# Kernel tuning notes

Hardware: AMD Instinct MI355X
Metric: run time of the kernel (lower is better)

The kernel has to match this reference:

```python
import jax, jax.numpy as jnp
import numpy as np

CHEB_K = 2  # chebyshev polynomial order (support_ks = [I, A] for cheb_k=2)


def _fc(x, w1, b1, w2, b2, w3, b3):
    # FC module: Linear -> sigmoid -> Linear -> sigmoid -> Linear
    h = jax.nn.sigmoid(x @ w1 + b1)
    h = jax.nn.sigmoid(h @ w2 + b2)
    return h @ w3 + b3


def _preprocess(adj):
    # adj: [B,N,N]; add self-loops then row-normalize
    adj = adj + jnp.eye(adj.shape[-1], dtype=adj.dtype)
    return adj / adj.sum(-1, keepdims=True)


def _gcn(x, adjs, ne, wpool, bpool):
    # x: [B,N,C], adjs: list of [B,N,N], ne: [N,E]
    # wpool: [E, 2*CHEB_K, C, O], bpool: [E, O]
    mats = []
    for A in adjs:
        ks = [jnp.broadcast_to(jnp.eye(A.shape[-1], dtype=A.dtype), A.shape), A]
        for _ in range(2, CHEB_K):
            ks.append(2.0 * jnp.matmul(A, ks[-1]) - ks[-2])
        mats.extend(ks)
    # [B,N,K,C] with K = 2*CHEB_K
    x_g = jnp.stack([jnp.einsum('bnm,bmc->bnc', S, x) for S in mats], axis=2)
    weights = jnp.einsum('nd,dkio->nkio', ne, wpool)  # [N,K,C,O]
    bias = ne @ bpool  # [N,O]
    return jnp.einsum('bnki,nkio->bno', x_g, weights) + bias


def _forward(x, state, ne0, ne1, ne2, fc1_w1, fc1_b1, fc1_w2, fc1_b2, fc1_w3, fc1_b3,
             fc2_w1, fc2_b1, fc2_w2, fc2_b2, fc2_w3, fc2_b3, gate_w, gate_b, upd_w, upd_b):
    hid = upd_w.shape[-1]
    ins = jnp.concatenate([x, state], axis=-1)  # [B,N,dim_in+hid]
    f1 = _fc(ins, fc1_w1, fc1_b1, fc1_w2, fc1_b2, fc1_w3, fc1_b3)  # [B,N,TD]
    f2 = _fc(ins, fc2_w1, fc2_b1, fc2_w2, fc2_b2, fc2_w3, fc2_b3)
    nv1 = jnp.tanh(ne0[:, None, :] * f1)  # einsum 'bd,bnd->bnd' == broadcast mul
    nv2 = jnp.tanh(ne1[:, None, :] * f2)
    adj = jnp.einsum('bnd,bmd->bnm', nv1, nv2) - jnp.einsum('bnd,bmd->bnm', nv2, nv1)
    adj1 = _preprocess(jax.nn.relu(adj))
    adj2 = _preprocess(jax.nn.relu(-jnp.swapaxes(adj, -2, -1)))
    z_r = jax.nn.sigmoid(_gcn(ins, [adj1, adj2], ne2, gate_w, gate_b))
    z, r = z_r[..., :hid], z_r[..., hid:]
    cand = jnp.concatenate([x, z * state], axis=-1)
    hc = jnp.tanh(_gcn(cand, [adj1, adj2], ne2, upd_w, upd_b))
    return r * state + (1.0 - r) * hc


def setup_inputs():
    B, N, DIN, DOUT, ED, TD = 32, 1024, 2, 64, 10, 32
    HG, MID = 16, 2  # hyperGNN_dim, middle_dim hardcoded in FC
    CIN = DIN + DOUT
    K2 = 2 * CHEB_K
    ks = jax.random.split(jax.random.key(0), 16)
    rn = lambda i, shape, s=1.0: jax.random.normal(ks[i], shape, dtype=jnp.float32) * s
    return {
        'x': rn(0, (B, N, DIN)),
        'state': rn(1, (B, N, DOUT)),
        'ne0': rn(2, (B, TD)),
        'ne1': rn(3, (B, TD)),
        'ne2': rn(4, (N, ED), 0.1),
        'fc1_w1': rn(5, (CIN, HG), 0.1), 'fc1_b1': jnp.zeros((HG,), jnp.float32),
        'fc1_w2': rn(6, (HG, MID), 0.1), 'fc1_b2': jnp.zeros((MID,), jnp.float32),
        'fc1_w3': rn(7, (MID, TD), 0.1), 'fc1_b3': jnp.zeros((TD,), jnp.float32),
        'fc2_w1': rn(8, (CIN, HG), 0.1), 'fc2_b1': jnp.zeros((HG,), jnp.float32),
        'fc2_w2': rn(9, (HG, MID), 0.1), 'fc2_b2': jnp.zeros((MID,), jnp.float32),
        'fc2_w3': rn(10, (MID, TD), 0.1), 'fc2_b3': jnp.zeros((TD,), jnp.float32),
        'gate_w': rn(11, (ED, K2, CIN, 2 * DOUT), 0.1),
        'gate_b': rn(12, (ED, 2 * DOUT), 0.1),
        'upd_w': rn(13, (ED, K2, CIN, DOUT), 0.1),
        'upd_b': rn(14, (ED, DOUT), 0.1),
    }


def reference(x, state, ne0, ne1, ne2, fc1_w1, fc1_b1, fc1_w2, fc1_b2, fc1_w3, fc1_b3,
              fc2_w1, fc2_b1, fc2_w2, fc2_b2, fc2_w3, fc2_b3, gate_w, gate_b, upd_w, upd_b):
    return _forward(x, state, ne0, ne1, ne2, fc1_w1, fc1_b1, fc1_w2, fc1_b2, fc1_w3, fc1_b3,
                    fc2_w1, fc2_b1, fc2_w2, fc2_b2, fc2_w3, fc2_b3, gate_w, gate_b, upd_w, upd_b)
```

## Files before the change

kernel.cpp:

```cpp
#include <hip/hip_runtime.h>
#include <math.h>

#define BB   32
#define NN   1024
#define DIN  2
#define DOUT 64
#define CIN  66
#define TD   32
#define ED   10
#define OG   128
#define OU   64
#define KP   160
#define XTR  80

typedef __bf16 bf16x8 __attribute__((ext_vector_type(8)));
typedef float  f32x4  __attribute__((ext_vector_type(4)));
typedef short  s16x8  __attribute__((ext_vector_type(8)));

__device__ __forceinline__ unsigned short f2b(float f) {
    __bf16 h = (__bf16)f;
    return *(unsigned short*)&h;
}

__device__ __forceinline__ unsigned int cvt_pk_bf16(float lo, float hi) {
    unsigned int r;
    asm("v_cvt_pk_bf16_f32 %0, %1, %2" : "=v"(r) : "v"(lo), "v"(hi));
    return r;
}
__device__ __forceinline__ void perm32swap(unsigned int& a, unsigned int& b) {
    asm("v_permlane32_swap_b32 %0, %1" : "+v"(a), "+v"(b));
}
__device__ __forceinline__ void perm16swap(unsigned int& a, unsigned int& b) {
    asm("v_permlane16_swap_b32 %0, %1" : "+v"(a), "+v"(b));
}

__global__ __launch_bounds__(256) void k_pre(
    const float* __restrict__ x, const float* __restrict__ state,
    const float* __restrict__ ne0, const float* __restrict__ ne1,
    const float* __restrict__ ne2,
    const float* __restrict__ w11, const float* __restrict__ b11,
    const float* __restrict__ w12, const float* __restrict__ b12,
    const float* __restrict__ w13, const float* __restrict__ b13,
    const float* __restrict__ w21, const float* __restrict__ b21,
    const float* __restrict__ w22, const float* __restrict__ b22,
    const float* __restrict__ w23, const float* __restrict__ b23,
    const float* __restrict__ gate_w, const float* __restrict__ gate_b,
    const float* __restrict__ upd_w, const float* __restrict__ upd_b,
    unsigned short* __restrict__ nv1b, unsigned short* __restrict__ nv2b,
    unsigned short* __restrict__ XT0, unsigned short* __restrict__ XT1,
    unsigned short* __restrict__ BcTg, unsigned short* __restrict__ BcTu,
    float* __restrict__ biasG, float* __restrict__ biasU)
{
    __shared__ float sw[2408];
    __shared__ unsigned short st[68*72];
    int blk = blockIdx.x;
    int t = threadIdx.x;

    if (blk < 128) {
        const int oW1 = 0, oB1 = 1056, oW2 = 1072, oB2 = 1104, oW3 = 1108, oB3 = 1172, F2 = 1204;
        for (int i = t; i < 1056; i += 256) { sw[oW1+i] = w11[i]; sw[F2+oW1+i] = w21[i]; }
        if (t < 16) { sw[oB1+t] = b11[t]; sw[F2+oB1+t] = b21[t]; }
        if (t < 32) { sw[oW2+t] = w12[t]; sw[F2+oW2+t] = w22[t]; }
        if (t < 2)  { sw[oB2+t] = b12[t]; sw[F2+oB2+t] = b22[t]; }
        if (t < 64) { sw[oW3+t] = w13[t]; sw[F2+oW3+t] = w23[t]; }
        if (t >= 64 && t < 96) { sw[oB3+t-64] = b13[t-64]; sw[F2+oB3+t-64] = b23[t-64]; }
        __syncthreads();

        int p = blk*256 + t;
        int b = p >> 10;

        float h1a[16], h1b[16];
        #pragma unroll
        for (int j = 0; j < 16; ++j) { h1a[j] = sw[oB1+j]; h1b[j] = sw[F2+oB1+j]; }
        for (int i = 0; i < CIN; ++i) {
            float v = (i < DIN) ? x[(size_t)p*DIN + i] : state[(size_t)p*DOUT + (i-DIN)];
            #pragma unroll
            for (int jq = 0; jq < 4; ++jq) {
                float4 wa = *(const float4*)&sw[oW1 + i*16 + jq*4];
                float4 wb = *(const float4*)&sw[F2 + oW1 + i*16 + jq*4];
                h1a[jq*4+0] += v*wa.x; h1a[jq*4+1] += v*wa.y;
                h1a[jq*4+2] += v*wa.z; h1a[jq*4+3] += v*wa.w;
                h1b[jq*4+0] += v*wb.x; h1b[jq*4+1] += v*wb.y;
                h1b[jq*4+2] += v*wb.z; h1b[jq*4+3] += v*wb.w;
            }
        }
        #pragma unroll
        for (int j = 0; j < 16; ++j) {
            h1a[j] = 1.f/(1.f + __expf(-h1a[j]));
            h1b[j] = 1.f/(1.f + __expf(-h1b[j]));
        }
        float h2a0 = sw[oB2+0], h2a1 = sw[oB2+1];
        float h2b0 = sw[F2+oB2+0], h2b1 = sw[F2+oB2+1];
        #pragma unroll
        for (int i = 0; i < 16; ++i) {
            h2a0 += h1a[i]*sw[oW2 + i*2 + 0];
            h2a1 += h1a[i]*sw[oW2 + i*2 + 1];
            h2b0 += h1b[i]*sw[F2+oW2 + i*2 + 0];
            h2b1 += h1b[i]*sw[F2+oW2 + i*2 + 1];
        }
        h2a0 = 1.f/(1.f + __expf(-h2a0)); h2a1 = 1.f/(1.f + __expf(-h2a1));
        h2b0 = 1.f/(1.f + __expf(-h2b0)); h2b1 = 1.f/(1.f + __expf(-h2b1));

        const float* pn0 = ne0 + b*TD;
        const float* pn1 = ne1 + b*TD;
        #pragma unroll
        for (int jq = 0; jq < 8; ++jq) {
            float4 ba  = *(const float4*)&sw[oB3 + jq*4];
            float4 wa0 = *(const float4*)&sw[oW3 + jq*4];
            float4 wa1 = *(const float4*)&sw[oW3 + 32 + jq*4];
            float4 bb2 = *(const float4*)&sw[F2+oB3 + jq*4];
            float4 wb0 = *(const float4*)&sw[F2+oW3 + jq*4];
            float4 wb1 = *(const float4*)&sw[F2+oW3 + 32 + jq*4];
            float4 n0 = *(const float4*)&pn0[jq*4];
            float4 n1 = *(const float4*)&pn1[jq*4];
            ushort4 u1, u2;
            u1.x = f2b(tanhf(n0.x*(ba.x + h2a0*wa0.x + h2a1*wa1.x)));
            u1.y = f2b(tanhf(n0.y*(ba.y + h2a0*wa0.y + h2a1*wa1.y)));
            u1.z = f2b(tanhf(n0.z*(ba.z + h2a0*wa0.z + h2a1*wa1.z)));
            u1.w = f2b(tanhf(n0.w*(ba.w + h2a0*wa0.w + h2a1*wa1.w)));
            u2.x = f2b(tanhf(n1.x*(bb2.x + h2b0*wb0.x + h2b1*wb1.x)));
            u2.y = f2b(tanhf(n1.y*(bb2.y + h2b0*wb0.y + h2b1*wb1.y)));
            u2.z = f2b(tanhf(n1.z*(bb2.z + h2b0*wb0.z + h2b1*wb1.z)));
            u2.w = f2b(tanhf(n1.w*(bb2.w + h2b0*wb0.w + h2b1*wb1.w)));
            *(ushort4*)&nv1b[(size_t)p*TD + jq*4] = u1;
            *(ushort4*)&nv2b[(size_t)p*TD + jq*4] = u2;
        }
    } else if (blk < 640) {
        int idx = blk - 128;
        int b = idx >> 4, m0 = (idx & 15)*64;
        for (int i = t; i < 1024; i += 256) {
            int m = i >> 4, cq = i & 15;
            size_t base = (size_t)b*NN + m0 + m;
            float4 v = *(const float4*)&state[base*DOUT + cq*4];
            st[(2 + cq*4 + 0)*72 + m] = f2b(v.x);
            st[(2 + cq*4 + 1)*72 + m] = f2b(v.y);
            st[(2 + cq*4 + 2)*72 + m] = f2b(v.z);
            st[(2 + cq*4 + 3)*72 + m] = f2b(v.w);
        }
        if (t < 128) {
            int m = t >> 1, c = t & 1;
            st[c*72 + m] = f2b(x[((size_t)b*NN + m0 + m)*DIN + c]);
        }
        __syncthreads();
        const unsigned int ONE2 = 0x3F803F80u;
        for (int i = t; i < XTR*8; i += 256) {
            int c = i >> 3, ch = i & 7;
            uint4 v;
            if (c < 66)      v = *(const uint4*)&st[c*72 + ch*8];
            else if (c == 66) v = make_uint4(ONE2, ONE2, ONE2, ONE2);
            else              v = make_uint4(0, 0, 0, 0);
            *(uint4*)&XT0[((size_t)b*XTR + c)*NN + m0 + ch*8] = v;
            if (c < 2 || c >= 66)
                *(uint4*)&XT1[((size_t)b*XTR + c)*NN + m0 + ch*8] = v;
        }
    } else if (blk < 1840) {
        int tid = (blk - 640)*256 + t;
        int c = tid / KP, k = tid - c*KP;
        const float* pool; int O, cc; unsigned short* dst;
        if (c < 1280) { pool = gate_w; O = OG; cc = c;        dst = BcTg; }
        else          { pool = upd_w;  O = OU; cc = c - 1280; dst = BcTu; }
        int d = cc / O, o = cc - d*O;
        float v = 0.f;
        if (k < 132) {
            int kp = (k < 66) ? 0 : 1;
            int i  = (k < 66) ? k : k - 66;
            v = pool[(size_t)((d*4 + kp)*CIN + i)*O + o]
              + pool[(size_t)((d*4 + kp + 2)*CIN + i)*O + o];
        }
        dst[(size_t)cc*KP + k] = f2b(v);
    } else {
        int i = (blk - 1840)*256 + t;
        int n = i / 192, j = i - n*192;
        float v = 0.f;
        if (j < 128) {
            #pragma unroll
            for (int d = 0; d < ED; ++d) v += ne2[(size_t)n*ED + d]*gate_b[d*OG + j];
            biasG[(size_t)n*OG + j] = v;
        } else {
            int o = j - 128;
            #pragma unroll
            for (int d = 0; d < ED; ++d) v += ne2[(size_t)n*ED + d]*upd_b[d*OU + o];
            biasU[(size_t)n*OU + o] = v;
        }
    }
}

template<int O, int MODE>
__global__ __launch_bounds__(256) void k_fused(
    const unsigned short* __restrict__ nv1b, const unsigned short* __restrict__ nv2b,
    const unsigned short* __restrict__ XTg, const unsigned short* __restrict__ BcT,
    const float* __restrict__ ne2, const float* __restrict__ biasP,
    const float* __restrict__ state, unsigned short* __restrict__ XT1,
    float* __restrict__ rbuf, float* __restrict__ out)
{
    __shared__ unsigned short smem[24192];
    unsigned short* s_nv1c = smem;
    unsigned short* s_nv2c = smem + 5120;
    unsigned short* s_xt   = smem + 10240;

    int t = threadIdx.x;
    int id = blockIdx.x;
    int b = id & 31, rbase = (id >> 5)*64;
    int w = t >> 6, lane = t & 63, lq = lane >> 4, ln = lane & 15;

    bf16x8 a1 = *(const bf16x8*)&nv1b[((size_t)b*NN + rbase + 16*w + ln)*TD + lq*8];
    s16x8 a2s = *(const s16x8*)&nv2b[((size_t)b*NN + rbase + 16*w + ln)*TD + lq*8];
    const s16x8 sgn = {(short)0x8000,(short)0x8000,(short)0x8000,(short)0x8000,
                       (short)0x8000,(short)0x8000,(short)0x8000,(short)0x8000};
    a2s ^= sgn;
    bf16x8 a2n = (bf16x8)a2s;

    const unsigned short* pnv1 = nv1b + (size_t)b*NN*TD;
    const unsigned short* pnv2 = nv2b + (size_t)b*NN*TD;
    const unsigned short* pxt  = XTg  + (size_t)b*XTR*NN;
    int nnode = t >> 2;
    int nch   = (t & 3)*8;
    int xc    = t >> 3;
    int xch   = (t & 7)*8;

    uint4 q0, q1, r0, r1, r2;

    f32x4 acc[5];
    #pragma unroll
    for (int k = 0; k < 5; ++k) acc[k] = (f32x4){0.f,0.f,0.f,0.f};
    const f32x4 zero4 = {0.f,0.f,0.f,0.f};
    union U8 { unsigned int u[4]; bf16x8 v; };

    q0 = *(const uint4*)&pnv1[(size_t)nnode*TD + nch];
    q1 = *(const uint4*)&pnv2[(size_t)nnode*TD + nch];
    r0 = *(const uint4*)&pxt[(size_t)xc*NN + xch];
    r1 = *(const uint4*)&pxt[(size_t)(xc+32)*NN + xch];
    if (t < 128) r2 = *(const uint4*)&pxt[(size_t)(xc+64)*NN + xch];
    *(uint4*)&s_nv1c[nnode*40 + nch] = q0;
    *(uint4*)&s_nv2c[nnode*40 + nch] = q1;
    *(uint4*)&s_xt[xc*72 + xch] = r0;
    *(uint4*)&s_xt[(xc+32)*72 + xch] = r1;
    if (t < 128) *(uint4*)&s_xt[(xc+64)*72 + xch] = r2;
    q0 = *(const uint4*)&pnv1[(size_t)(64 + nnode)*TD + nch];
    q1 = *(const uint4*)&pnv2[(size_t)(64 + nnode)*TD + nch];
    r0 = *(const uint4*)&pxt[(size_t)xc*NN + 64 + xch];
    r1 = *(const uint4*)&pxt[(size_t)(xc+32)*NN + 64 + xch];
    if (t < 128) r2 = *(const uint4*)&pxt[(size_t)(xc+64)*NN + 64 + xch];
    __syncthreads();

    int cur = 0;
    for (int mb = 0; mb < NN; mb += 64) {
        if (mb + 64 < NN) {
            int nx = cur ^ 1;
            *(uint4*)&s_nv1c[nx*2560 + nnode*40 + nch] = q0;
            *(uint4*)&s_nv2c[nx*2560 + nnode*40 + nch] = q1;
            *(uint4*)&s_xt[nx*5760 + xc*72 + xch] = r0;
            *(uint4*)&s_xt[nx*5760 + (xc+32)*72 + xch] = r1;
            if (t < 128) *(uint4*)&s_xt[nx*5760 + (xc+64)*72 + xch] = r2;
        }
        if (mb + 128 < NN) {
            int mb2 = mb + 128;
            q0 = *(const uint4*)&pnv1[(size_t)(mb2 + nnode)*TD + nch];
            q1 = *(const uint4*)&pnv2[(size_t)(mb2 + nnode)*TD + nch];
            r0 = *(const uint4*)&pxt[(size_t)xc*NN + mb2 + xch];
            r1 = *(const uint4*)&pxt[(size_t)(xc+32)*NN + mb2 + xch];
            if (t < 128) r2 = *(const uint4*)&pxt[(size_t)(xc+64)*NN + mb2 + xch];
        }

        unsigned int u[4][2];
        #pragma unroll
        for (int jj = 0; jj < 4; ++jj) {
            bf16x8 b2 = *(const bf16x8*)&s_nv2c[cur*2560 + (jj*16 + ln)*40 + lq*8];
            bf16x8 b1 = *(const bf16x8*)&s_nv1c[cur*2560 + (jj*16 + ln)*40 + lq*8];
            f32x4 s = __builtin_amdgcn_mfma_f32_16x16x32_bf16(b2, a1,  zero4, 0, 0, 0);
            s       = __builtin_amdgcn_mfma_f32_16x16x32_bf16(b1, a2n, s,     0, 0, 0);
            u[jj][0] = cvt_pk_bf16(fmaxf(s[0], 0.f), fmaxf(s[1], 0.f));
            u[jj][1] = cvt_pk_bf16(fmaxf(s[2], 0.f), fmaxf(s[3], 0.f));
        }

        unsigned int w00 = u[0][0], w20 = u[1][0]; perm32swap(w00, w20); perm16swap(w00, w20);
        unsigned int w01 = u[0][1], w21 = u[1][1]; perm32swap(w01, w21); perm16swap(w01, w21);
        unsigned int x00 = u[2][0], x20 = u[3][0]; perm32swap(x00, x20); perm16swap(x00, x20);
        unsigned int x01 = u[2][1], x21 = u[3][1]; perm32swap(x01, x21); perm16swap(x01, x21);
        U8 p0, p1;
        p0.u[0] = w00; p0.u[1] = w01; p0.u[2] = w20; p0.u[3] = w21;
        p1.u[0] = x00; p1.u[1] = x01; p1.u[2] = x20; p1.u[3] = x21;
        bf16x8 pa0 = p0.v, pa1 = p1.v;

        #pragma unroll
        for (int k = 0; k < 5; ++k) {
            bf16x8 xb0 = *(const bf16x8*)&s_xt[cur*5760 + (k*16 + ln)*72 +      lq*8];
            bf16x8 xb1 = *(const bf16x8*)&s_xt[cur*5760 + (k*16 + ln)*72 + 32 + lq*8];
            acc[k] = __builtin_amdgcn_mfma_f32_16x16x32_bf16(pa0, xb0, acc[k], 0, 0, 0);
            acc[k] = __builtin_amdgcn_mfma_f32_16x16x32_bf16(pa1, xb1, acc[k], 0, 0, 0);
        }

        __syncthreads();
        cur ^= 1;
    }

    float rinv[4];
    #pragma unroll
    for (int r = 0; r < 4; ++r) {
        float rs = __shfl(acc[4][r], (lane & 48) | 2, 64);
        rinv[r] = 1.0f / (1.0f + rs);
    }

    unsigned short* s_A = smem;
    unsigned short* s_B = smem + 10752;

    for (int i = t; i < 64*28; i += 256) {
        int rr = i / 28, cc = 132 + (i - 28*(i/28));
        s_A[rr*168 + cc] = 0;
    }
    #pragma unroll
    for (int k = 0; k < 5; ++k) {
        int c = k*16 + ln;
        if (c < CIN) {
            #pragma unroll
            for (int r = 0; r < 4; ++r) {
                int row_l = 16*w + lq*4 + r;
                int gr = rbase + row_l;
                unsigned short xu = XTg[((size_t)b*XTR + c)*NN + gr];
                float xr = (float)(*(const __bf16*)&xu);
                s_A[row_l*168 + c]      = xu;
                s_A[row_l*168 + 66 + c] = f2b((acc[k][r] + xr) * rinv[r]);
            }
        }
    }

    for (int ot = 0; ot < O/16; ++ot) {
        int o0 = ot*16, o = o0 + ln;
        float part[4];
        f32x4 gac[5];

        #pragma unroll
        for (int h = 0; h < 2; ++h) {
            __syncthreads();
            for (int i = t; i < 1600; i += 256) {
                int cc = i / 20, kc = i - cc*20;
                int d = h*5 + (cc >> 4), oo = cc & 15;
                *(uint4*)&s_B[cc*168 + kc*8] =
                    *(const uint4*)&BcT[(size_t)(d*O + o0 + oo)*KP + kc*8];
            }
            #pragma unroll
            for (int c = 0; c < 5; ++c) gac[c] = (f32x4){0.f,0.f,0.f,0.f};
            __syncthreads();

            #pragma unroll
            for (int kc = 0; kc < 5; ++kc) {
                bf16x8 af = *(const bf16x8*)&s_A[(16*w + ln)*168 + kc*32 + lq*8];
                #pragma unroll
                for (int ct = 0; ct < 5; ++ct) {
                    bf16x8 bf = *(const bf16x8*)&s_B[(ct*16 + ln)*168 + kc*32 + lq*8];
                    gac[ct] = __builtin_amdgcn_mfma_f32_16x16x32_bf16(af, bf, gac[ct], 0, 0, 0);
                }
            }

            #pragma unroll
            for (int r = 0; r < 4; ++r) {
                int row_l = 16*w + lq*4 + r;
                int n = rbase + row_l;
                size_t rowG = (size_t)b*NN + n;
                const float* nep = &ne2[(size_t)n*ED];
                float val = (h == 0) ? biasP[(size_t)n*O + o] : part[r];
                #pragma unroll
                for (int d = 0; d < 5; ++d) val += nep[h*5 + d] * gac[d][r];
                if (h == 0) {
                    part[r] = val;
                } else {
                    if (MODE == 0) {
                        float sv = 1.f/(1.f + __expf(-val));
                        if (o < 64) {
                            float zst = sv * state[rowG*DOUT + o];
                            XT1[((size_t)b*XTR + 2 + o)*NN + n] = f2b(zst);
                        } else {
                            rbuf[rowG*DOUT + (o - 64)] = sv;
                        }
                    } else {
                        float hc = tanhf(val);
                        float rg = rbuf[rowG*DOUT + o];
                        float st = state[rowG*DOUT + o];
                        out[rowG*DOUT + o] = rg*st + (1.f - rg)*hc;
                    }
                }
            }
        }
    }
}

extern "C" void kernel_launch(void* const* d_in, const int* in_sizes, int n_in,
                              void* d_out, int out_size, void* d_ws, size_t ws_size,
                              hipStream_t stream)
{
    const float* x      = (const float*)d_in[0];
    const float* state  = (const float*)d_in[1];
    const float* ne0    = (const float*)d_in[2];
    const float* ne1    = (const float*)d_in[3];
    const float* ne2    = (const float*)d_in[4];
    const float* f1w1   = (const float*)d_in[5];
    const float* f1b1   = (const float*)d_in[6];
    const float* f1w2   = (const float*)d_in[7];
    const float* f1b2   = (const float*)d_in[8];
    const float* f1w3   = (const float*)d_in[9];
    const float* f1b3   = (const float*)d_in[10];
    const float* f2w1   = (const float*)d_in[11];
    const float* f2b1   = (const float*)d_in[12];
    const float* f2w2   = (const float*)d_in[13];
    const float* f2b2   = (const float*)d_in[14];
    const float* f2w3   = (const float*)d_in[15];
    const float* f2b3   = (const float*)d_in[16];
    const float* gate_w = (const float*)d_in[17];
    const float* gate_b = (const float*)d_in[18];
    const float* upd_w  = (const float*)d_in[19];
    const float* upd_b  = (const float*)d_in[20];

    unsigned short* nv1b = (unsigned short*)d_ws;
    unsigned short* nv2b = nv1b + (size_t)BB*NN*TD;
    unsigned short* XT0  = nv2b + (size_t)BB*NN*TD;
    unsigned short* XT1  = XT0  + (size_t)BB*XTR*NN;
    unsigned short* BcTg = XT1  + (size_t)BB*XTR*NN;
    unsigned short* BcTu = BcTg + (size_t)1280*KP;
    float* biasG = (float*)(BcTu + (size_t)640*KP);
    float* biasU = biasG + (size_t)NN*OG;
    float* rbuf  = biasU + (size_t)NN*OU;
    float* out   = (float*)d_out;

    k_pre<<<dim3(2608), 256, 0, stream>>>(x, state, ne0, ne1, ne2,
        f1w1, f1b1, f1w2, f1b2, f1w3, f1b3,
        f2w1, f2b1, f2w2, f2b2, f2w3, f2b3,
        gate_w, gate_b, upd_w, upd_b,
        nv1b, nv2b, XT0, XT1, BcTg, BcTu, biasG, biasU);

    k_fused<OG,0><<<dim3(512), 256, 0, stream>>>(nv1b, nv2b, XT0, BcTg, ne2,
                                                 biasG, state, XT1, rbuf, nullptr);

    k_fused<OU,1><<<dim3(512), 256, 0, stream>>>(nv1b, nv2b, XT1, BcTu, ne2,
                                                 biasU, state, nullptr, rbuf, out);
}
```

Measured before the change: 230.3 us.

## Double-buffer weight tiles in LDS with register prefetch in fused GCN kernel

Replaces the per-tile load-sync-compute loop over weight tiles with a double-buffered LDS scheme. The next tile is written from registers while the current one is consumed, and the tile after that is prefetched from global memory into registers. The A fragments and the ne2 rows are also hoisted into registers once, so they are no longer reloaded for every tile. This cuts barriers to one per half-tile and hides global-load latency, at the cost of more LDS (about 75KB) and more registers, which may reduce occupancy.

Result: slower. 298.1 us (+29.5%).

```diff
diff --git a/kernel.cpp b/kernel.cpp
--- a/kernel.cpp
+++ b/kernel.cpp
@@ -32,6 +32,32 @@
 }
 __device__ __forceinline__ void perm16swap(unsigned int& a, unsigned int& b) {
     asm("v_permlane16_swap_b32 %0, %1" : "+v"(a), "+v"(b));
+}
+
+__device__ __forceinline__ void loadB(
+    const unsigned short* __restrict__ BcT, int O, int o0, int h, int t,
+    uint4 (&pr)[7])
+{
+    #pragma unroll
+    for (int k = 0; k < 7; ++k) {
+        int i = k*256 + t;
+        if (i < 1600) {
+            int cc = i/20, kc = i - cc*20;
+            int d = h*5 + (cc >> 4), oo = cc & 15;
+            pr[k] = *(const uint4*)&BcT[(size_t)(d*O + o0 + oo)*KP + kc*8];
+        }
+    }
+}
+__device__ __forceinline__ void writeB(unsigned short* sb, int t, const uint4 (&pr)[7])
+{
+    #pragma unroll
+    for (int k = 0; k < 7; ++k) {
+        int i = k*256 + t;
+        if (i < 1600) {
+            int cc = i/20, kc = i - cc*20;
+            *(uint4*)&sb[cc*168 + kc*8] = pr[k];
+        }
+    }
 }
 
 __global__ __launch_bounds__(256) void k_pre(
@@ -193,7 +219,7 @@
     const float* __restrict__ state, unsigned short* __restrict__ XT1,
     float* __restrict__ rbuf, float* __restrict__ out)
 {
-    __shared__ unsigned short smem[24192];
+    __shared__ unsigned short smem[37632];
     unsigned short* s_nv1c = smem;
     unsigned short* s_nv2c = smem + 5120;
     unsigned short* s_xt   = smem + 10240;
@@ -324,63 +350,78 @@
         }
     }
 
-    for (int ot = 0; ot < O/16; ++ot) {
-        int o0 = ot*16, o = o0 + ln;
-        float part[4];
+    for (int i = t; i < 1600; i += 256) {
+        int cc = i/20, kc = i - cc*20;
+        int d = (cc >> 4), oo = cc & 15;
+        *(uint4*)&s_B[cc*168 + kc*8] = *(const uint4*)&BcT[(size_t)(d*O + oo)*KP + kc*8];
+    }
+    uint4 pr[7];
+    loadB(BcT, O, 0, 1, t, pr);
+    __syncthreads();
+
+    bf16x8 af[5];
+    #pragma unroll
+    for (int kc = 0; kc < 5; ++kc)
+        af[kc] = *(const bf16x8*)&s_A[(16*w + ln)*168 + kc*32 + lq*8];
+    float nepr[4][10];
+    #pragma unroll
+    for (int r = 0; r < 4; ++r) {
+        int n = rbase + 16*w + lq*4 + r;
+        #pragma unroll
+        for (int d = 0; d < 10; ++d) nepr[r][d] = ne2[(size_t)n*ED + d];
+    }
+
+    const int NH = (O/16)*2;
+    int gcur = 0;
+    float part[4];
+    for (int hh = 0; hh < NH; ++hh) {
+        int h = hh & 1, o0 = (hh >> 1)*16, o = o0 + ln;
+
+        if (hh + 1 < NH) writeB(s_B + (gcur^1)*13440, t, pr);
+        if (hh + 2 < NH) loadB(BcT, O, ((hh+2) >> 1)*16, (hh+2) & 1, t, pr);
+
         f32x4 gac[5];
-
-        #pragma unroll
-        for (int h = 0; h < 2; ++h) {
-            __syncthreads();
-            for (int i = t; i < 1600; i += 256) {
-                int cc = i / 20, kc = i - cc*20;
-                int d = h*5 + (cc >> 4), oo = cc & 15;
-                *(uint4*)&s_B[cc*168 + kc*8] =
-                    *(const uint4*)&BcT[(size_t)(d*O + o0 + oo)*KP + kc*8];
+        #pragma unroll
+        for (int c = 0; c < 5; ++c) gac[c] = (f32x4){0.f,0.f,0.f,0.f};
+        const unsigned short* sb = s_B + gcur*13440;
+        #pragma unroll
+        for (int kc = 0; kc < 5; ++kc) {
+            #pragma unroll
+            for (int ct = 0; ct < 5; ++ct) {
+                bf16x8 bf = *(const bf16x8*)&sb[(ct*16 + ln)*168 + kc*32 + lq*8];
+                gac[ct] = __builtin_amdgcn_mfma_f32_16x16x32_bf16(af[kc], bf, gac[ct], 0, 0, 0);
             }
-            #pragma unroll
-            for (int c = 0; c < 5; ++c) gac[c] = (f32x4){0.f,0.f,0.f,0.f};
-            __syncthreads();
-
-            #pragma unroll
-            for (int kc = 0; kc < 5; ++kc) {
-                bf16x8 af = *(const bf16x8*)&s_A[(16*w + ln)*168 + kc*32 + lq*8];
-                #pragma unroll
-                for (int ct = 0; ct < 5; ++ct) {
-                    bf16x8 bf = *(const bf16x8*)&s_B[(ct*16 + ln)*168 + kc*32 + lq*8];
-                    gac[ct] = __builtin_amdgcn_mfma_f32_16x16x32_bf16(af, bf, gac[ct], 0, 0, 0);
+        }
+
+        #pragma unroll
+        for (int r = 0; r < 4; ++r) {
+            int row_l = 16*w + lq*4 + r;
+            int n = rbase + row_l;
+            size_t rowG = (size_t)b*NN + n;
+            float val = (h == 0) ? biasP[(size_t)n*O + o] : part[r];
+            #pragma unroll
+            for (int d = 0; d < 5; ++d) val += nepr[r][h*5 + d] * gac[d][r];
+            if (h == 0) {
+                part[r] = val;
+            } else {
+                if (MODE == 0) {
+                    float sv = 1.f/(1.f + __expf(-val));
+                    if (o < 64) {
+                        float zst = sv * state[rowG*DOUT + o];
+                        XT1[((size_t)b*XTR + 2 + o)*NN + n] = f2b(zst);
+                    } else {
+                        rbuf[rowG*DOUT + (o - 64)] = sv;
+                    }
+                } else {
+                    float hc = tanhf(val);
+                    float rg = rbuf[rowG*DOUT + o];
+                    float st = state[rowG*DOUT + o];
+                    out[rowG*DOUT + o] = rg*st + (1.f - rg)*hc;
                 }
             }
-
-            #pragma unroll
-            for (int r = 0; r < 4; ++r) {
-                int row_l = 16*w + lq*4 + r;
-                int n = rbase + row_l;
-                size_t rowG = (size_t)b*NN + n;
-                const float* nep = &ne2[(size_t)n*ED];
-                float val = (h == 0) ? biasP[(size_t)n*O + o] : part[r];
-                #pragma unroll
-                for (int d = 0; d < 5; ++d) val += nep[h*5 + d] * gac[d][r];
-                if (h == 0) {
-                    part[r] = val;
-                } else {
-                    if (MODE == 0) {
-                        float sv = 1.f/(1.f + __expf(-val));
-                        if (o < 64) {
-                            float zst = sv * state[rowG*DOUT + o];
-                            XT1[((size_t)b*XTR + 2 + o)*NN + n] = f2b(zst);
-                        } else {
-                            rbuf[rowG*DOUT + (o - 64)] = sv;
-                        }
-                    } else {
-                        float hc = tanhf(val);
-                        float rg = rbuf[rowG*DOUT + o];
-                        float st = state[rowG*DOUT + o];
-                        out[rowG*DOUT + o] = rg*st + (1.f - rg)*hc;
-                    }
-                }
-            }
-        }
+        }
+        __syncthreads();
+        gcur ^= 1;
     }
 }
 
```
